# Kernel tuning notes

Measured on AMD Instinct MI355X. Metric: run time of the kernel, lower is better.

The kernel has to match this reference:

```python
import jax, jax.numpy as jnp
import numpy as np

EPS = 1e-08


def setup_inputs() -> dict:
    key = jax.random.key(0)
    k1, k2 = jax.random.split(key)
    N, D, C = 8192, 512, 1000
    features = jax.random.uniform(k1, (N, D), dtype=jnp.float32)
    logits = jax.random.normal(k2, (N, C), dtype=jnp.float32)
    return {"features": features, "logits": logits}


def reference(features, logits):
    N = features.shape[0]
    # softmax over classes, plus eps (matches F.softmax(...) + eps)
    p = jax.nn.softmax(logits, axis=1) + EPS                     # [N, C]
    # similarity matrix with diagonal removed
    cos_sim = features @ features.T - jnp.eye(N, dtype=features.dtype)  # [N, N]
    neighbor_mask = (cos_sim >= -1).astype(cos_sim.dtype)
    w = cos_sim * neighbor_mask
    w = w / jnp.sum(w, axis=1, keepdims=True)                    # row-normalized weights
    weighted_sum_nb = w @ p                                      # [N, C]
    # F.kl_div(log_input, target, reduction='batchmean')
    # = sum(target * (log(target) - log_input)) / N
    kl = jnp.sum(weighted_sum_nb * (jnp.log(weighted_sum_nb) - jnp.log(p))) / N
    return kl
```

## Files before the change

### kernel.cpp

```cpp
#include <hip/hip_runtime.h>
#include <math.h>

#define NN 8192
#define DD 512
#define CC 1000
#define CP 1024

typedef __attribute__((ext_vector_type(8))) short short8;
typedef __attribute__((ext_vector_type(4))) float f32x4;
typedef __attribute__((ext_vector_type(4))) unsigned short us4;
typedef __attribute__((ext_vector_type(8))) unsigned short us8;
typedef __attribute__((ext_vector_type(4))) unsigned int ui4;

__device__ __forceinline__ float bf2f(unsigned short u){
  union{unsigned int i; float f;} v; v.i = ((unsigned int)u)<<16; return v.f;
}
__device__ __forceinline__ unsigned short f2bf(float f){
  union{float f; unsigned int i;} v; v.f = f;
  unsigned int r = v.i + 0x7FFF + ((v.i>>16)&1);
  return (unsigned short)(r>>16);
}
__device__ __forceinline__ float waveRedSum(float v){
  #pragma unroll
  for(int o=32;o;o>>=1) v += __shfl_xor(v,o,64);
  return v;
}
__device__ __forceinline__ float waveRedMax(float v){
  #pragma unroll
  for(int o=32;o;o>>=1) v = fmaxf(v,__shfl_xor(v,o,64));
  return v;
}
__device__ __forceinline__ void gload_lds16(const void* g, void* l){
  __builtin_amdgcn_global_load_lds((const __attribute__((address_space(1))) void*)g,
                                   (__attribute__((address_space(3))) void*)l, 16, 0, 0);
}

__global__ __launch_bounds__(256) void k_castF(const float* __restrict__ F,
                                               unsigned short* __restrict__ FbT,
                                               unsigned short* __restrict__ Fb,
                                               float* __restrict__ gpart){
  __shared__ unsigned short lds[64*68];
  __shared__ float gq[16*64];
  int t = threadIdx.x;
  int i0 = blockIdx.x*64, d0 = blockIdx.y*64;
  int cx = t&15, ry = t>>4;
  float ca0=0.f,ca1=0.f,ca2=0.f,ca3=0.f;
  #pragma unroll
  for(int rr=0;rr<4;rr++){
    int row = rr*16 + ry;
    f32x4 fv = *(const f32x4*)&F[(size_t)(i0+row)*DD + d0 + cx*4];
    us4 u; u[0]=f2bf(fv[0]); u[1]=f2bf(fv[1]); u[2]=f2bf(fv[2]); u[3]=f2bf(fv[3]);
    *(us4*)&lds[row*68 + cx*4] = u;
    *(us4*)&Fb[(size_t)(i0+row)*DD + d0 + cx*4] = u;
    ca0+=fv[0]; ca1+=fv[1]; ca2+=fv[2]; ca3+=fv[3];
  }
  {
    f32x4 cv; cv[0]=ca0; cv[1]=ca1; cv[2]=ca2; cv[3]=ca3;
    *(f32x4*)&gq[ry*64 + cx*4] = cv;
  }
  __syncthreads();
  #pragma unroll
  for(int rr=0;rr<4;rr++){
    int d = rr*16 + ry;
    us4 u;
    #pragma unroll
    for(int q=0;q<4;q++) u[q] = lds[(cx*4+q)*68 + d];
    *(us4*)&FbT[(size_t)(d0+d)*NN + i0 + cx*4] = u;
  }
  __syncthreads();
  if(t<64){
    float s=0.f;
    #pragma unroll
    for(int j=0;j<16;j++) s += gq[j*64+t];
    gpart[blockIdx.x*DD + d0 + t] = s;
  }
}

__global__ __launch_bounds__(256) void k_gred(const float* __restrict__ gpart,
                                              float* __restrict__ g){
  __shared__ float rs[4][64];
  int t = threadIdx.x;
  int d = blockIdx.x*64 + (t&63);
  int q = t>>6;
  float s = 0.f;
  #pragma unroll
  for(int j=0;j<32;j++) s += gpart[(size_t)(q*32+j)*DD + d];
  rs[q][t&63] = s;
  __syncthreads();
  if(q==0) g[d] = rs[0][t&63]+rs[1][t&63]+rs[2][t&63]+rs[3][t&63];
}

__global__ __launch_bounds__(256) void k_softmaxT(const float* __restrict__ L,
                                                  unsigned short* __restrict__ PbT){
  __shared__ unsigned int lt[8][1028];
  int t = threadIdx.x, l = t&63, w = t>>6;
  int i0 = blockIdx.x*16;
  #pragma unroll
  for(int q=0;q<4;q++){
    int rr = w*4 + q;
    int row = i0 + rr;
    const float* lr = L + (size_t)row*CC;
    float v[16]; float mx = -1e30f;
    #pragma unroll
    for(int k=0;k<16;k++){ int c = l + 64*k; v[k] = (c<CC)? lr[c] : -1e30f; mx = fmaxf(mx,v[k]); }
    mx = waveRedMax(mx);
    float s = 0.f;
    #pragma unroll
    for(int k=0;k<16;k++){ v[k] = expf(v[k]-mx); s += v[k]; }
    s = waveRedSum(s);
    float inv = 1.0f/s;
    #pragma unroll
    for(int k=0;k<16;k++){
      int c = l + 64*k;
      float p = v[k]*inv + 1e-8f;
      unsigned short h = (c<CC)? f2bf(p) : (unsigned short)0;
      *((unsigned short*)&lt[rr>>1][c] + (rr&1)) = h;
    }
  }
  __syncthreads();
  #pragma unroll
  for(int k=0;k<4;k++){
    int c = t + 256*k;
    ui4 a, b;
    #pragma unroll
    for(int j=0;j<4;j++){ a[j] = lt[j][c]; b[j] = lt[j+4][c]; }
    *(ui4*)&PbT[(size_t)c*NN + i0]     = a;
    *(ui4*)&PbT[(size_t)c*NN + i0 + 8] = b;
  }
}

__global__ __launch_bounds__(256,2) void k_gemm1(const unsigned short* __restrict__ A,
                                                 const unsigned short* __restrict__ B,
                                                 unsigned short* __restrict__ Tpb){
  __shared__ unsigned short Al[128*64];
  __shared__ unsigned short Bl[128*64];
  int t = threadIdx.x, l = t&63, w = t>>6;
  int m0 = blockIdx.x*128, n0 = blockIdx.y*128;
  int k0 = blockIdx.z*512;
  int wm = w>>1, wn = w&1;
  f32x4 acc[4][4] = {};
  int srow = w*32 + (l>>3);
  int scl  = (l&7) ^ (srow&7);
  const unsigned short* Ab = A + (size_t)(m0 + srow)*NN + k0 + scl*8;
  const unsigned short* Bb = B + (size_t)(n0 + srow)*NN + k0 + scl*8;
  unsigned short* AlB = Al + (w*32)*64;
  unsigned short* BlB = Bl + (w*32)*64;

  for(int kt=0; kt<512; kt+=64){
    __syncthreads();
    #pragma unroll
    for(int q=0;q<4;q++){
      gload_lds16(Ab + (size_t)q*8*NN + kt, AlB + q*8*64);
      gload_lds16(Bb + (size_t)q*8*NN + kt, BlB + q*8*64);
    }
    asm volatile("s_waitcnt vmcnt(0)" ::: "memory");
    __syncthreads();
    #pragma unroll
    for(int ks=0;ks<2;ks++){
      short8 af[4], bf[4];
      #pragma unroll
      for(int mi=0;mi<4;mi++){
        int r = wm*64 + mi*16 + (l&15);
        int ch = ((ks<<2) + (l>>4)) ^ (r&7);
        af[mi] = *(const short8*)&Al[r*64 + ch*8];
      }
      #pragma unroll
      for(int ni=0;ni<4;ni++){
        int r = wn*64 + ni*16 + (l&15);
        int ch = ((ks<<2) + (l>>4)) ^ (r&7);
        bf[ni] = *(const short8*)&Bl[r*64 + ch*8];
      }
      #pragma unroll
      for(int mi=0;mi<4;mi++)
        #pragma unroll
        for(int ni=0;ni<4;ni++)
          acc[mi][ni] = __builtin_amdgcn_mfma_f32_16x16x32_bf16(af[mi], bf[ni], acc[mi][ni], 0,0,0);
    }
  }
  unsigned short* Tz = Tpb + (size_t)blockIdx.z*CP*DD;
  int rbase = (l>>4)*4;
  #pragma unroll
  for(int mi=0;mi<4;mi++){
    int c = m0 + wm*64 + mi*16 + rbase;
    #pragma unroll
    for(int ni=0;ni<4;ni++){
      int d = n0 + wn*64 + ni*16 + (l&15);
      #pragma unroll
      for(int j=0;j<4;j++)
        Tz[(size_t)(c+j)*DD + d] = f2bf(acc[mi][ni][j]);
    }
  }
}

__global__ __launch_bounds__(256) void k_redT(const unsigned short* __restrict__ Tpb,
                                              const unsigned short* __restrict__ Fb,
                                              const float* __restrict__ g,
                                              unsigned short* __restrict__ Ttb,
                                              float* __restrict__ invr){
  int t = threadIdx.x;
  size_t i = ((size_t)blockIdx.x*256 + (size_t)t)*8;
  f32x4 s0 = {0.f,0.f,0.f,0.f}, s1 = {0.f,0.f,0.f,0.f};
  #pragma unroll
  for(int z=0;z<16;z++){
    us8 v = *(const us8*)&Tpb[(size_t)z*CP*DD + i];
    s0[0]+=bf2f(v[0]); s0[1]+=bf2f(v[1]); s0[2]+=bf2f(v[2]); s0[3]+=bf2f(v[3]);
    s1[0]+=bf2f(v[4]); s1[1]+=bf2f(v[5]); s1[2]+=bf2f(v[6]); s1[3]+=bf2f(v[7]);
  }
  us8 u;
  u[0]=f2bf(s0[0]); u[1]=f2bf(s0[1]); u[2]=f2bf(s0[2]); u[3]=f2bf(s0[3]);
  u[4]=f2bf(s1[0]); u[5]=f2bf(s1[1]); u[6]=f2bf(s1[2]); u[7]=f2bf(s1[3]);
  *(us8*)&Ttb[i] = u;
  int row = blockIdx.x*32 + (t>>3);
  int seg = (t&7)*64;
  const unsigned short* fr = Fb + (size_t)row*DD + seg;
  const float* gr = g + seg;
  float s = 0.f;
  #pragma unroll
  for(int j=0;j<8;j++){
    us8 f8 = *(const us8*)&fr[j*8];
    f32x4 ga = *(const f32x4*)&gr[j*8];
    f32x4 gb = *(const f32x4*)&gr[j*8+4];
    s += bf2f(f8[0])*ga[0]+bf2f(f8[1])*ga[1]+bf2f(f8[2])*ga[2]+bf2f(f8[3])*ga[3]
       + bf2f(f8[4])*gb[0]+bf2f(f8[5])*gb[1]+bf2f(f8[6])*gb[2]+bf2f(f8[7])*gb[3];
  }
  s += __shfl_xor(s,1,64); s += __shfl_xor(s,2,64); s += __shfl_xor(s,4,64);
  if((t&7)==0) invr[row] = 1.0f/(s - 1.0f);
}

__global__ __launch_bounds__(256,2) void k_gemm2(const unsigned short* __restrict__ Fb,
                                                 const unsigned short* __restrict__ Bt,
                                                 const unsigned short* __restrict__ PbT,
                                                 const float* __restrict__ invr,
                                                 float* __restrict__ partials){
  __shared__ unsigned short Al[128*64];
  __shared__ unsigned short Bl[128*64];
  __shared__ float red[4];
  int t = threadIdx.x, l = t&63, w = t>>6;
  int m0 = blockIdx.y*128, n0 = blockIdx.x*128;
  int wm = w>>1, wn = w&1;
  f32x4 acc[4][4] = {};
  int srow = w*32 + (l>>3);
  int scl  = (l&7) ^ (srow&7);
  const unsigned short* Ab = Fb + (size_t)(m0 + srow)*DD + scl*8;
  const unsigned short* Bb = Bt + (size_t)(n0 + srow)*DD + scl*8;
  unsigned short* AlB = Al + (w*32)*64;
  unsigned short* BlB = Bl + (w*32)*64;

  for(int kt=0; kt<512; kt+=64){
    __syncthreads();
    #pragma unroll
    for(int q=0;q<4;q++){
      gload_lds16(Ab + (size_t)q*8*DD + kt, AlB + q*8*64);
      gload_lds16(Bb + (size_t)q*8*DD + kt, BlB + q*8*64);
    }
    asm volatile("s_waitcnt vmcnt(0)" ::: "memory");
    __syncthreads();
    #pragma unroll
    for(int ks=0;ks<2;ks++){
      short8 af[4], bf[4];
      #pragma unroll
      for(int mi=0;mi<4;mi++){
        int r = wm*64 + mi*16 + (l&15);
        int ch = ((ks<<2) + (l>>4)) ^ (r&7);
        af[mi] = *(const short8*)&Al[r*64 + ch*8];
      }
      #pragma unroll
      for(int ni=0;ni<4;ni++){
        int r = wn*64 + ni*16 + (l&15);
        int ch = ((ks<<2) + (l>>4)) ^ (r&7);
        bf[ni] = *(const short8*)&Bl[r*64 + ch*8];
      }
      #pragma unroll
      for(int mi=0;mi<4;mi++)
        #pragma unroll
        for(int ni=0;ni<4;ni++)
          acc[mi][ni] = __builtin_amdgcn_mfma_f32_16x16x32_bf16(af[mi], bf[ni], acc[mi][ni], 0,0,0);
    }
  }
  float kl = 0.f;
  int rbase = (l>>4)*4;
  #pragma unroll
  for(int mi=0;mi<4;mi++){
    int i_base = m0 + wm*64 + mi*16 + rbase;
    f32x4 ir4 = *(const f32x4*)&invr[i_base];
    #pragma unroll
    for(int ni=0;ni<4;ni++){
      int c = n0 + wn*64 + ni*16 + (l&15);
      if(c < CC){
        us4 p4 = *(const us4*)&PbT[(size_t)c*NN + i_base];
        #pragma unroll
        for(int j=0;j<4;j++){
          float p = bf2f(p4[j]);
          float ws = (acc[mi][ni][j] - p) * ir4[j];
          kl += ws * logf(ws/p);
        }
      }
    }
  }
  kl = waveRedSum(kl);
  if(l==0) red[w]=kl;
  __syncthreads();
  if(t==0) partials[blockIdx.y*8 + blockIdx.x] = red[0]+red[1]+red[2]+red[3];
}

__global__ __launch_bounds__(64) void k_finalize(const float* __restrict__ partials,
                                                 float* __restrict__ out){
  int l = threadIdx.x;
  double s = 0.0;
  for(int j=l; j<512; j+=64) s += (double)partials[j];
  #pragma unroll
  for(int o=32;o;o>>=1) s += __shfl_xor(s,o,64);
  if(l==0) out[0] = (float)(s / (double)NN);
}

extern "C" void kernel_launch(void* const* d_in, const int* in_sizes, int n_in,
                              void* d_out, int out_size, void* d_ws, size_t ws_size,
                              hipStream_t stream){
  const float* F = (const float*)d_in[0];
  const float* L = (const float*)d_in[1];
  float* out = (float*)d_out;

  unsigned char* w8 = (unsigned char*)d_ws;
  unsigned short* FbT = (unsigned short*)w8;
  unsigned short* PbT = (unsigned short*)(w8 + (8u<<20));
  unsigned short* Tpb = (unsigned short*)(w8 + (24u<<20));
  unsigned short* Ttb = (unsigned short*)(w8 + (40u<<20));
  unsigned short* Fb  = (unsigned short*)(w8 + (41u<<20));
  float* gpart        = (float*)(w8 + (49u<<20));
  float* g            = (float*)(w8 + (49u<<20) + 262144);
  float* invr         = (float*)(w8 + (49u<<20) + 264192);
  float* partials     = (float*)(w8 + (49u<<20) + 296960);

  hipLaunchKernelGGL(k_castF,    dim3(128,8),  dim3(256), 0, stream, F, FbT, Fb, gpart);
  hipLaunchKernelGGL(k_gred,     dim3(8),      dim3(256), 0, stream, gpart, g);
  hipLaunchKernelGGL(k_softmaxT, dim3(512),    dim3(256), 0, stream, L, PbT);
  hipLaunchKernelGGL(k_gemm1,    dim3(8,4,16), dim3(256), 0, stream, PbT, FbT, Tpb);
  hipLaunchKernelGGL(k_redT,     dim3(256),    dim3(256), 0, stream, Tpb, Fb, g, Ttb, invr);
  hipLaunchKernelGGL(k_gemm2,    dim3(8,64),   dim3(256), 0, stream, Fb, Ttb, PbT, invr, partials);
  hipLaunchKernelGGL(k_finalize, dim3(1),      dim3(64),  0, stream, partials, out);
}
```

Before: 77.61 us.

## Merge cast and softmax prep kernels; fold column-sum reduce into gemm1 launch

Combines the feature cast/transpose kernel and the softmax-transpose kernel into one launch that interleaves their blocks (two cast blocks per softmax block). It also appends the column-sum reduction blocks to the gemm1 grid as extra blocks, cutting the launch count from seven to five and letting independent work share the GPU. It also switches to fast __expf/__logf intrinsics, replacing logf of a ratio with a difference of two logs, at a small accuracy risk. Shared memory in the prep kernel grows to the larger of the two layouts, which may lower occupancy for the cast blocks.

```diff
diff --git a/kernel.cpp b/kernel.cpp
--- a/kernel.cpp
+++ b/kernel.cpp
@@ -35,108 +35,120 @@
                                    (__attribute__((address_space(3))) void*)l, 16, 0, 0);
 }
 
-__global__ __launch_bounds__(256) void k_castF(const float* __restrict__ F,
-                                               unsigned short* __restrict__ FbT,
-                                               unsigned short* __restrict__ Fb,
-                                               float* __restrict__ gpart){
-  __shared__ unsigned short lds[64*68];
-  __shared__ float gq[16*64];
+__global__ __launch_bounds__(256) void k_prep(const float* __restrict__ F,
+                                              const float* __restrict__ L,
+                                              unsigned short* __restrict__ FbT,
+                                              unsigned short* __restrict__ Fb,
+                                              float* __restrict__ gpart,
+                                              unsigned short* __restrict__ PbT){
+  __shared__ __align__(16) char smem[8*1028*4];
+  int bid = blockIdx.x;
+  int grp = bid/3, r = bid - grp*3;
   int t = threadIdx.x;
-  int i0 = blockIdx.x*64, d0 = blockIdx.y*64;
-  int cx = t&15, ry = t>>4;
-  float ca0=0.f,ca1=0.f,ca2=0.f,ca3=0.f;
-  #pragma unroll
-  for(int rr=0;rr<4;rr++){
-    int row = rr*16 + ry;
-    f32x4 fv = *(const f32x4*)&F[(size_t)(i0+row)*DD + d0 + cx*4];
-    us4 u; u[0]=f2bf(fv[0]); u[1]=f2bf(fv[1]); u[2]=f2bf(fv[2]); u[3]=f2bf(fv[3]);
-    *(us4*)&lds[row*68 + cx*4] = u;
-    *(us4*)&Fb[(size_t)(i0+row)*DD + d0 + cx*4] = u;
-    ca0+=fv[0]; ca1+=fv[1]; ca2+=fv[2]; ca3+=fv[3];
-  }
-  {
-    f32x4 cv; cv[0]=ca0; cv[1]=ca1; cv[2]=ca2; cv[3]=ca3;
-    *(f32x4*)&gq[ry*64 + cx*4] = cv;
-  }
-  __syncthreads();
-  #pragma unroll
-  for(int rr=0;rr<4;rr++){
-    int d = rr*16 + ry;
-    us4 u;
-    #pragma unroll
-    for(int q=0;q<4;q++) u[q] = lds[(cx*4+q)*68 + d];
-    *(us4*)&FbT[(size_t)(d0+d)*NN + i0 + cx*4] = u;
-  }
-  __syncthreads();
-  if(t<64){
-    float s=0.f;
-    #pragma unroll
-    for(int j=0;j<16;j++) s += gq[j*64+t];
-    gpart[blockIdx.x*DD + d0 + t] = s;
-  }
-}
-
-__global__ __launch_bounds__(256) void k_gred(const float* __restrict__ gpart,
-                                              float* __restrict__ g){
-  __shared__ float rs[4][64];
-  int t = threadIdx.x;
-  int d = blockIdx.x*64 + (t&63);
-  int q = t>>6;
-  float s = 0.f;
-  #pragma unroll
-  for(int j=0;j<32;j++) s += gpart[(size_t)(q*32+j)*DD + d];
-  rs[q][t&63] = s;
-  __syncthreads();
-  if(q==0) g[d] = rs[0][t&63]+rs[1][t&63]+rs[2][t&63]+rs[3][t&63];
-}
-
-__global__ __launch_bounds__(256) void k_softmaxT(const float* __restrict__ L,
-                                                  unsigned short* __restrict__ PbT){
-  __shared__ unsigned int lt[8][1028];
-  int t = threadIdx.x, l = t&63, w = t>>6;
-  int i0 = blockIdx.x*16;
-  #pragma unroll
-  for(int q=0;q<4;q++){
-    int rr = w*4 + q;
-    int row = i0 + rr;
-    const float* lr = L + (size_t)row*CC;
-    float v[16]; float mx = -1e30f;
-    #pragma unroll
-    for(int k=0;k<16;k++){ int c = l + 64*k; v[k] = (c<CC)? lr[c] : -1e30f; mx = fmaxf(mx,v[k]); }
-    mx = waveRedMax(mx);
-    float s = 0.f;
-    #pragma unroll
-    for(int k=0;k<16;k++){ v[k] = expf(v[k]-mx); s += v[k]; }
-    s = waveRedSum(s);
-    float inv = 1.0f/s;
-    #pragma unroll
-    for(int k=0;k<16;k++){
-      int c = l + 64*k;
-      float p = v[k]*inv + 1e-8f;
-      unsigned short h = (c<CC)? f2bf(p) : (unsigned short)0;
-      *((unsigned short*)&lt[rr>>1][c] + (rr&1)) = h;
-    }
-  }
-  __syncthreads();
-  #pragma unroll
-  for(int k=0;k<4;k++){
-    int c = t + 256*k;
-    ui4 a, b;
-    #pragma unroll
-    for(int j=0;j<4;j++){ a[j] = lt[j][c]; b[j] = lt[j+4][c]; }
-    *(ui4*)&PbT[(size_t)c*NN + i0]     = a;
-    *(ui4*)&PbT[(size_t)c*NN + i0 + 8] = b;
+
+  if(r < 2){
+    int cb = grp*2 + r;
+    unsigned short* lds = (unsigned short*)smem;
+    float* gq = (float*)(smem + 64*68*2);
+    int i0 = (cb & 127)*64, d0 = (cb >> 7)*64;
+    int cx = t&15, ry = t>>4;
+    float ca0=0.f,ca1=0.f,ca2=0.f,ca3=0.f;
+    #pragma unroll
+    for(int rr=0;rr<4;rr++){
+      int row = rr*16 + ry;
+      f32x4 fv = *(const f32x4*)&F[(size_t)(i0+row)*DD + d0 + cx*4];
+      us4 u; u[0]=f2bf(fv[0]); u[1]=f2bf(fv[1]); u[2]=f2bf(fv[2]); u[3]=f2bf(fv[3]);
+      *(us4*)&lds[row*68 + cx*4] = u;
+      *(us4*)&Fb[(size_t)(i0+row)*DD + d0 + cx*4] = u;
+      ca0+=fv[0]; ca1+=fv[1]; ca2+=fv[2]; ca3+=fv[3];
+    }
+    {
+      f32x4 cv; cv[0]=ca0; cv[1]=ca1; cv[2]=ca2; cv[3]=ca3;
+      *(f32x4*)&gq[ry*64 + cx*4] = cv;
+    }
+    __syncthreads();
+    #pragma unroll
+    for(int rr=0;rr<4;rr++){
+      int d = rr*16 + ry;
+      us4 u;
+      #pragma unroll
+      for(int q=0;q<4;q++) u[q] = lds[(cx*4+q)*68 + d];
+      *(us4*)&FbT[(size_t)(d0+d)*NN + i0 + cx*4] = u;
+    }
+    __syncthreads();
+    if(t<64){
+      float s=0.f;
+      #pragma unroll
+      for(int j=0;j<16;j++) s += gq[j*64+t];
+      gpart[cb&127 ? (cb&127)*DD + d0 + t : d0 + t] = s;
+    }
+  } else {
+    int sb = grp;
+    unsigned int (*lt)[1028] = (unsigned int(*)[1028])smem;
+    int l = t&63, w = t>>6;
+    int i0 = sb*16;
+    #pragma unroll
+    for(int q=0;q<4;q++){
+      int rr = w*4 + q;
+      int row = i0 + rr;
+      const float* lr = L + (size_t)row*CC;
+      float v[16]; float mx = -1e30f;
+      #pragma unroll
+      for(int k=0;k<16;k++){ int c = l + 64*k; v[k] = (c<CC)? lr[c] : -1e30f; mx = fmaxf(mx,v[k]); }
+      mx = waveRedMax(mx);
+      float s = 0.f;
+      #pragma unroll
+      for(int k=0;k<16;k++){ v[k] = __expf(v[k]-mx); s += v[k]; }
+      s = waveRedSum(s);
+      float inv = 1.0f/s;
+      #pragma unroll
+      for(int k=0;k<16;k++){
+        int c = l + 64*k;
+        float p = v[k]*inv + 1e-8f;
+        unsigned short h = (c<CC)? f2bf(p) : (unsigned short)0;
+        *((unsigned short*)&lt[rr>>1][c] + (rr&1)) = h;
+      }
+    }
+    __syncthreads();
+    #pragma unroll
+    for(int k=0;k<4;k++){
+      int c = t + 256*k;
+      ui4 a, b;
+      #pragma unroll
+      for(int j=0;j<4;j++){ a[j] = lt[j][c]; b[j] = lt[j+4][c]; }
+      *(ui4*)&PbT[(size_t)c*NN + i0]     = a;
+      *(ui4*)&PbT[(size_t)c*NN + i0 + 8] = b;
+    }
   }
 }
 
 __global__ __launch_bounds__(256,2) void k_gemm1(const unsigned short* __restrict__ A,
                                                  const unsigned short* __restrict__ B,
-                                                 unsigned short* __restrict__ Tpb){
+                                                 unsigned short* __restrict__ Tpb,
+                                                 const float* __restrict__ gpart,
+                                                 float* __restrict__ g){
   __shared__ unsigned short Al[128*64];
   __shared__ unsigned short Bl[128*64];
-  int t = threadIdx.x, l = t&63, w = t>>6;
-  int m0 = blockIdx.x*128, n0 = blockIdx.y*128;
-  int k0 = blockIdx.z*512;
+  __shared__ float rs[4][64];
+  int bid = blockIdx.x;
+  int t = threadIdx.x;
+  if(bid >= 512){
+    int gb = bid - 512;
+    int d = gb*64 + (t&63);
+    int q = t>>6;
+    float s = 0.f;
+    #pragma unroll
+    for(int j=0;j<32;j++) s += gpart[(size_t)(q*32+j)*DD + d];
+    rs[q][t&63] = s;
+    __syncthreads();
+    if(q==0) g[d] = rs[0][t&63]+rs[1][t&63]+rs[2][t&63]+rs[3][t&63];
+    return;
+  }
+  int l = t&63, w = t>>6;
+  int bx = bid & 7, byz = bid >> 3;
+  int by = byz & 3, bz = byz >> 2;
+  int m0 = bx*128, n0 = by*128;
+  int k0 = bz*512;
   int wm = w>>1, wn = w&1;
   f32x4 acc[4][4] = {};
   int srow = w*32 + (l>>3);
@@ -160,15 +172,15 @@
       short8 af[4], bf[4];
       #pragma unroll
       for(int mi=0;mi<4;mi++){
-        int r = wm*64 + mi*16 + (l&15);
-        int ch = ((ks<<2) + (l>>4)) ^ (r&7);
-        af[mi] = *(const short8*)&Al[r*64 + ch*8];
+        int rr = wm*64 + mi*16 + (l&15);
+        int ch = ((ks<<2) + (l>>4)) ^ (rr&7);
+        af[mi] = *(const short8*)&Al[rr*64 + ch*8];
       }
       #pragma unroll
       for(int ni=0;ni<4;ni++){
-        int r = wn*64 + ni*16 + (l&15);
-        int ch = ((ks<<2) + (l>>4)) ^ (r&7);
-        bf[ni] = *(const short8*)&Bl[r*64 + ch*8];
+        int rr = wn*64 + ni*16 + (l&15);
+        int ch = ((ks<<2) + (l>>4)) ^ (rr&7);
+        bf[ni] = *(const short8*)&Bl[rr*64 + ch*8];
       }
       #pragma unroll
       for(int mi=0;mi<4;mi++)
@@ -177,7 +189,7 @@
           acc[mi][ni] = __builtin_amdgcn_mfma_f32_16x16x32_bf16(af[mi], bf[ni], acc[mi][ni], 0,0,0);
     }
   }
-  unsigned short* Tz = Tpb + (size_t)blockIdx.z*CP*DD;
+  unsigned short* Tz = Tpb + (size_t)bz*CP*DD;
   int rbase = (l>>4)*4;
   #pragma unroll
   for(int mi=0;mi<4;mi++){
@@ -260,15 +272,15 @@
       short8 af[4], bf[4];
       #pragma unroll
       for(int mi=0;mi<4;mi++){
-        int r = wm*64 + mi*16 + (l&15);
-        int ch = ((ks<<2) + (l>>4)) ^ (r&7);
-        af[mi] = *(const short8*)&Al[r*64 + ch*8];
+        int rr = wm*64 + mi*16 + (l&15);
+        int ch = ((ks<<2) + (l>>4)) ^ (rr&7);
+        af[mi] = *(const short8*)&Al[rr*64 + ch*8];
       }
       #pragma unroll
       for(int ni=0;ni<4;ni++){
-        int r = wn*64 + ni*16 + (l&15);
-        int ch = ((ks<<2) + (l>>4)) ^ (r&7);
-        bf[ni] = *(const short8*)&Bl[r*64 + ch*8];
+        int rr = wn*64 + ni*16 + (l&15);
+        int ch = ((ks<<2) + (l>>4)) ^ (rr&7);
+        bf[ni] = *(const short8*)&Bl[rr*64 + ch*8];
       }
       #pragma unroll
       for(int mi=0;mi<4;mi++)
@@ -292,7 +304,7 @@
         for(int j=0;j<4;j++){
           float p = bf2f(p4[j]);
           float ws = (acc[mi][ni][j] - p) * ir4[j];
-          kl += ws * logf(ws/p);
+          kl += ws * (__logf(ws) - __logf(p));
         }
       }
     }
@@ -331,10 +343,8 @@
   float* invr         = (float*)(w8 + (49u<<20) + 264192);
   float* partials     = (float*)(w8 + (49u<<20) + 296960);
 
-  hipLaunchKernelGGL(k_castF,    dim3(128,8),  dim3(256), 0, stream, F, FbT, Fb, gpart);
-  hipLaunchKernelGGL(k_gred,     dim3(8),      dim3(256), 0, stream, gpart, g);
-  hipLaunchKernelGGL(k_softmaxT, dim3(512),    dim3(256), 0, stream, L, PbT);
-  hipLaunchKernelGGL(k_gemm1,    dim3(8,4,16), dim3(256), 0, stream, PbT, FbT, Tpb);
+  hipLaunchKernelGGL(k_prep,     dim3(1536),   dim3(256), 0, stream, F, L, FbT, Fb, gpart, PbT);
+  hipLaunchKernelGGL(k_gemm1,    dim3(520),    dim3(256), 0, stream, PbT, FbT, Tpb, gpart, g);
   hipLaunchKernelGGL(k_redT,     dim3(256),    dim3(256), 0, stream, Tpb, Fb, g, Ttb, invr);
   hipLaunchKernelGGL(k_gemm2,    dim3(8,64),   dim3(256), 0, stream, Fb, Ttb, PbT, invr, partials);
   hipLaunchKernelGGL(k_finalize, dim3(1),      dim3(64),  0, stream, partials, out);
```

After: 73.74 us. 1.05x faster.
